# Kernel optimization log

Hardware: AMD Instinct MI355X
Metric: run time of the kernel (lower is better)

Reference implementation:

```python
import jax, jax.numpy as jnp
import numpy as np

# DPLayer config (init kwargs)
MAX_OP = False            # False -> min-plus (shortest path) semiring; null = +inf
MAKE_POS = True           # GraphLayer make_pos: force positive edge weights
NULL = -1e30 if MAX_OP else 1e30   # finite stand-in for +/-inf (grad-safe)
B, H, W = 512, 256, 256


def setup_inputs() -> dict:
    key = jax.random.key(0)
    images = jax.random.normal(key, (B, 1, H, W), dtype=jnp.float32)
    return {"images": images}


def _edge_weights(images):
    # GraphLayer: edge_f('euclidean') on pixel values, made positive via softplus.
    x = images[:, 0, :, :]                       # [B, H, W] node/edge costs theta
    if MAKE_POS:
        x = jax.nn.softplus(x)
    return x


def _dp(theta):
    # V[i,j] = theta[i,j] + comb(V[i-1,j], V[i-1,j-1], V[i,j-1]); comb = min (max_op=False)
    # Row recurrence is solved in parallel via prefix-sum + associative running-min:
    #   A[j] = comb(V[i-1,j], V[i-1,j-1])
    #   V[i,j] = S[j] + runmin_{k<=j}(A[k] - S[k-1]),  S = cumsum(theta row)
    comb = jnp.maximum if MAX_OP else jnp.minimum
    null = jnp.asarray(NULL, theta.dtype)
    b = theta.shape[0]

    v0 = jnp.cumsum(theta[:, 0, :], axis=-1)     # first row: only right moves

    def row_step(vprev, th_row):                 # vprev: [B,W], th_row: [B,W]
        shifted = jnp.concatenate([jnp.full((b, 1), null, theta.dtype), vprev[:, :-1]], axis=1)
        A = comb(vprev, shifted)                 # best of up / up-left
        S = jnp.cumsum(th_row, axis=-1)
        Sprev = jnp.concatenate([jnp.zeros((b, 1), theta.dtype), S[:, :-1]], axis=1)
        V = S + jax.lax.associative_scan(comb, A - Sprev, axis=-1)
        return V, None

    vlast, _ = jax.lax.scan(row_step, v0, jnp.moveaxis(theta[:, 1:, :], 1, 0))
    return vlast[:, -1]                          # path length to (H-1, W-1), [B]


def reference(images):
    theta = _edge_weights(images)
    fake_lengths = _dp(theta)
    return fake_lengths
```

## Files before the change

kernel.cpp:

```cpp
#include <hip/hip_runtime.h>


#define HH 256
#define WW 256
#define CH 16
#define NCH 16
#define NULLV 1e30f

template<int CTRL, int ROWM>
__device__ __forceinline__ float dpp_mov(float x, float oldv) {
    return __builtin_bit_cast(float, __builtin_amdgcn_update_dpp(
        __builtin_bit_cast(int, oldv), __builtin_bit_cast(int, x),
        CTRL, ROWM, 0xF, false));
}

__device__ __forceinline__ float wave_iscan_min(float x) {
    asm volatile(
        "s_nop 1\n\t"
        "v_min_f32_dpp %0, %0, %0 row_shr:1  row_mask:0xf bank_mask:0xf\n\t"
        "s_nop 1\n\t"
        "v_min_f32_dpp %0, %0, %0 row_shr:2  row_mask:0xf bank_mask:0xf\n\t"
        "s_nop 1\n\t"
        "v_min_f32_dpp %0, %0, %0 row_shr:4  row_mask:0xf bank_mask:0xf\n\t"
        "s_nop 1\n\t"
        "v_min_f32_dpp %0, %0, %0 row_shr:8  row_mask:0xf bank_mask:0xf\n\t"
        "s_nop 1\n\t"
        "v_min_f32_dpp %0, %0, %0 row_bcast:15 row_mask:0xa bank_mask:0xf\n\t"
        "s_nop 1\n\t"
        "v_min_f32_dpp %0, %0, %0 row_bcast:31 row_mask:0xc bank_mask:0xf"
        : "+v"(x));
    return x;
}

__device__ __forceinline__ float wave_iscan_add(float x) {
    asm volatile(
        "s_nop 1\n\t"
        "v_add_f32_dpp %0, %0, %0 row_shr:1  row_mask:0xf bank_mask:0xf bound_ctrl:0\n\t"
        "s_nop 1\n\t"
        "v_add_f32_dpp %0, %0, %0 row_shr:2  row_mask:0xf bank_mask:0xf bound_ctrl:0\n\t"
        "s_nop 1\n\t"
        "v_add_f32_dpp %0, %0, %0 row_shr:4  row_mask:0xf bank_mask:0xf bound_ctrl:0\n\t"
        "s_nop 1\n\t"
        "v_add_f32_dpp %0, %0, %0 row_shr:8  row_mask:0xf bank_mask:0xf bound_ctrl:0\n\t"
        "s_nop 1\n\t"
        "v_add_f32_dpp %0, %0, %0 row_bcast:15 row_mask:0xa bank_mask:0xf bound_ctrl:0\n\t"
        "s_nop 1\n\t"
        "v_add_f32_dpp %0, %0, %0 row_bcast:31 row_mask:0xc bank_mask:0xf bound_ctrl:0"
        : "+v"(x));
    return x;
}

__device__ __forceinline__ float softplus_f(float x) {
    float ax = fabsf(x);
    float t  = __expf(-ax);
    return fmaxf(x, 0.0f) + __logf(1.0f + t);
}

__device__ __forceinline__ float4 prep_row(float4 c) {
    float t0 = softplus_f(c.x);
    float t1 = t0 + softplus_f(c.y);
    float t2 = t1 + softplus_f(c.z);
    float t3 = t2 + softplus_f(c.w);
    float s    = wave_iscan_add(t3);
    float soff = dpp_mov<0x138, 0xF>(s, 0.0f);
    return make_float4(soff + t0, soff + t1, soff + t2, soff + t3);
}

template<int NR>
__device__ __forceinline__ void load_rows(const float4* gp, int r0, float4* L) {
#pragma unroll
    for (int i = 0; i < NR; ++i) L[i] = gp[(size_t)(r0 + i) * 64];
}

template<int NR>
__device__ __forceinline__ void prep_store(const float4* L, float* dst, int lane) {
#pragma unroll
    for (int i = 0; i < NR; ++i)
        *reinterpret_cast<float4*>(&dst[i * WW + lane * 4]) = prep_row(L[i]);
}

template<int NR>
__device__ __forceinline__ void prep_run(const float4* gp, int row0,
                                         float* base0, float* base1, int lane) {
    float4 L[NR];
    load_rows<NR>(gp, CH + row0, L);
    __syncthreads();
    for (int k = 1; k < NCH; ++k) {
        float4 N[NR];
        if (k + 1 < NCH) load_rows<NR>(gp, (k + 1) * CH + row0, N);
        prep_store<NR>(L, (k & 1) ? base1 : base0, lane);
        __syncthreads();
        if (k + 1 < NCH) {
#pragma unroll
            for (int i = 0; i < NR; ++i) L[i] = N[i];
        }
    }
}

__global__ __launch_bounds__(512, 1) void dp_kernel(const float* __restrict__ img,
                                                    float* __restrict__ out) {
    const int tid = threadIdx.x;
    const int wid = tid >> 6;
    const int lane = tid & 63;

    __shared__ __align__(16) float sbuf[2][2][CH][WW];

    const int imgi = (wid < 2) ? wid : ((wid - 2) & 1);
    const float* gbase = img + (size_t)(2 * blockIdx.x + imgi) * HH * WW;
    const float4* gp = reinterpret_cast<const float4*>(gbase) + lane;

    if (wid < 2) {
        {
            float4 C[4];
            load_rows<4>(gp, 0, C);
            prep_store<4>(C, &sbuf[imgi][0][0][0], lane);
        }
        __syncthreads();
        __builtin_amdgcn_s_setprio(1);

        float v0, v1, v2, v3;
        auto row_step = [&](const float4& S) {
            float soff = dpp_mov<0x138, 0xF>(S.w, 0.0f);
            float vm1  = dpp_mov<0x138, 0xF>(v3, NULLV);
            float B0 = fminf(v0, vm1) - soff;
            float B1 = fminf(v1, v0) - S.x;
            float B2 = fminf(v2, v1) - S.y;
            float B3 = fminf(v3, v2) - S.z;
            float m1 = fminf(B0, B1);
            float p  = fminf(B2, B3);
            float m2 = fminf(m1, B2);
            float m3 = fminf(m1, p);
            float mm   = wave_iscan_min(m3);
            float moff = dpp_mov<0x138, 0xF>(mm, NULLV);
            v0 = S.x + fminf(moff, B0);
            v1 = S.y + fminf(moff, m1);
            v2 = S.z + fminf(moff, m2);
            v3 = S.w + fminf(moff, m3);
        };

#define RD8(P, buf, r0)                                                  \
    P##0 = *reinterpret_cast<const float4*>(&(buf)[(r0) + 0][lane * 4]); \
    P##1 = *reinterpret_cast<const float4*>(&(buf)[(r0) + 1][lane * 4]); \
    P##2 = *reinterpret_cast<const float4*>(&(buf)[(r0) + 2][lane * 4]); \
    P##3 = *reinterpret_cast<const float4*>(&(buf)[(r0) + 3][lane * 4]); \
    P##4 = *reinterpret_cast<const float4*>(&(buf)[(r0) + 4][lane * 4]); \
    P##5 = *reinterpret_cast<const float4*>(&(buf)[(r0) + 5][lane * 4]); \
    P##6 = *reinterpret_cast<const float4*>(&(buf)[(r0) + 6][lane * 4]); \
    P##7 = *reinterpret_cast<const float4*>(&(buf)[(r0) + 7][lane * 4]);
#define ST8(P)                                                           \
    row_step(P##0); row_step(P##1); row_step(P##2); row_step(P##3);      \
    row_step(P##4); row_step(P##5); row_step(P##6); row_step(P##7);

        float4 A0, A1, A2, A3, A4, A5, A6, A7;
        float4 B0, B1, B2, B3, B4, B5, B6, B7;

        {
            const float(*buf)[WW] = sbuf[imgi][0];
            RD8(A, buf, 0); RD8(B, buf, 8);
            v0 = A0.x; v1 = A0.y; v2 = A0.z; v3 = A0.w;
            row_step(A1); row_step(A2); row_step(A3);
            row_step(A4); row_step(A5); row_step(A6); row_step(A7);
            ST8(B);
        }
        for (int k = 1; k < NCH; ++k) {
            __syncthreads();
            const float(*buf)[WW] = sbuf[imgi][k & 1];
            RD8(A, buf, 0); RD8(B, buf, 8);
            ST8(A);
            ST8(B);
        }
#undef RD8
#undef ST8
        if (lane == 63) out[2 * blockIdx.x + imgi] = v3;
    } else {
        const int pw = (wid - 2) >> 1;
        {
            float4 C[4];
            load_rows<4>(gp, 4 + 4 * pw, C);
            prep_store<4>(C, &sbuf[imgi][0][4 + 4 * pw][0], lane);
        }
        const int row0 = (pw == 0) ? 0 : (pw == 1) ? 6 : 11;
        float* b0 = &sbuf[imgi][0][row0][0];
        float* b1 = &sbuf[imgi][1][row0][0];
        if (pw == 0) prep_run<6>(gp, row0, b0, b1, lane);
        else         prep_run<5>(gp, row0, b0, b1, lane);
    }
}

extern "C" void kernel_launch(void* const* d_in, const int* in_sizes, int n_in,
                              void* d_out, int out_size, void* d_ws, size_t ws_size,
                              hipStream_t stream) {
    const float* img = (const float*)d_in[0];
    float* out = (float*)d_out;
    dp_kernel<<<out_size / 2, 512, 0, stream>>>(img, out);
}
```

Measured before the change: 39.94 us.

## Process one image per block with six producer waves and two blocks per CU

Restructures the kernel so each block handles a single image with one DP wave (wave 3) and six softplus/prefix-sum producer waves, instead of two images with two DP waves and six producers. Shared memory is halved and launch bounds change to 448 threads with 2 blocks per CU, doubling the grid. The intent is finer-grained scheduling and more producer throughput per DP wave so the serial row recurrence is less starved. The cost is more blocks, more barriers per image, and possible register pressure under the tighter occupancy bound.

Result: faster. 38.43 us (median of 2 runs) (-3.8%).

```diff
diff --git a/kernel.cpp b/kernel.cpp
--- a/kernel.cpp
+++ b/kernel.cpp
@@ -97,23 +97,22 @@
     }
 }
 
-__global__ __launch_bounds__(512, 1) void dp_kernel(const float* __restrict__ img,
+__global__ __launch_bounds__(448, 2) void dp_kernel(const float* __restrict__ img,
                                                     float* __restrict__ out) {
     const int tid = threadIdx.x;
     const int wid = tid >> 6;
     const int lane = tid & 63;
 
-    __shared__ __align__(16) float sbuf[2][2][CH][WW];
+    __shared__ __align__(16) float sbuf[2][CH][WW];
 
-    const int imgi = (wid < 2) ? wid : ((wid - 2) & 1);
-    const float* gbase = img + (size_t)(2 * blockIdx.x + imgi) * HH * WW;
+    const float* gbase = img + (size_t)blockIdx.x * HH * WW;
     const float4* gp = reinterpret_cast<const float4*>(gbase) + lane;
 
-    if (wid < 2) {
+    if (wid == 3) {
         {
-            float4 C[4];
-            load_rows<4>(gp, 0, C);
-            prep_store<4>(C, &sbuf[imgi][0][0][0], lane);
+            float4 C[2];
+            load_rows<2>(gp, 0, C);
+            prep_store<2>(C, &sbuf[0][0][0], lane);
         }
         __syncthreads();
         __builtin_amdgcn_s_setprio(1);
@@ -155,7 +154,7 @@
         float4 B0, B1, B2, B3, B4, B5, B6, B7;
 
         {
-            const float(*buf)[WW] = sbuf[imgi][0];
+            const float(*buf)[WW] = sbuf[0];
             RD8(A, buf, 0); RD8(B, buf, 8);
             v0 = A0.x; v1 = A0.y; v2 = A0.z; v3 = A0.w;
             row_step(A1); row_step(A2); row_step(A3);
@@ -164,26 +163,28 @@
         }
         for (int k = 1; k < NCH; ++k) {
             __syncthreads();
-            const float(*buf)[WW] = sbuf[imgi][k & 1];
+            const float(*buf)[WW] = sbuf[k & 1];
             RD8(A, buf, 0); RD8(B, buf, 8);
             ST8(A);
             ST8(B);
         }
 #undef RD8
 #undef ST8
-        if (lane == 63) out[2 * blockIdx.x + imgi] = v3;
+        if (lane == 63) out[blockIdx.x] = v3;
     } else {
-        const int pw = (wid - 2) >> 1;
-        {
-            float4 C[4];
-            load_rows<4>(gp, 4 + 4 * pw, C);
-            prep_store<4>(C, &sbuf[imgi][0][4 + 4 * pw][0], lane);
-        }
-        const int row0 = (pw == 0) ? 0 : (pw == 1) ? 6 : 11;
-        float* b0 = &sbuf[imgi][0][row0][0];
-        float* b1 = &sbuf[imgi][1][row0][0];
-        if (pw == 0) prep_run<6>(gp, row0, b0, b1, lane);
-        else         prep_run<5>(gp, row0, b0, b1, lane);
+        if (wid == 0) { float4 C[3]; load_rows<3>(gp,  2, C); prep_store<3>(C, &sbuf[0][ 2][0], lane); }
+        else if (wid == 1) { float4 C[3]; load_rows<3>(gp,  5, C); prep_store<3>(C, &sbuf[0][ 5][0], lane); }
+        else if (wid == 2) { float4 C[3]; load_rows<3>(gp,  8, C); prep_store<3>(C, &sbuf[0][ 8][0], lane); }
+        else if (wid == 4) { float4 C[2]; load_rows<2>(gp, 11, C); prep_store<2>(C, &sbuf[0][11][0], lane); }
+        else if (wid == 5) { float4 C[2]; load_rows<2>(gp, 13, C); prep_store<2>(C, &sbuf[0][13][0], lane); }
+        else               { float4 C[1]; load_rows<1>(gp, 15, C); prep_store<1>(C, &sbuf[0][15][0], lane); }
+
+        if (wid == 0)      prep_run<3>(gp,  0, &sbuf[0][ 0][0], &sbuf[1][ 0][0], lane);
+        else if (wid == 1) prep_run<3>(gp,  3, &sbuf[0][ 3][0], &sbuf[1][ 3][0], lane);
+        else if (wid == 2) prep_run<3>(gp,  6, &sbuf[0][ 6][0], &sbuf[1][ 6][0], lane);
+        else if (wid == 4) prep_run<3>(gp,  9, &sbuf[0][ 9][0], &sbuf[1][ 9][0], lane);
+        else if (wid == 5) prep_run<2>(gp, 12, &sbuf[0][12][0], &sbuf[1][12][0], lane);
+        else               prep_run<2>(gp, 14, &sbuf[0][14][0], &sbuf[1][14][0], lane);
     }
 }
 
@@ -192,5 +193,5 @@
                               hipStream_t stream) {
     const float* img = (const float*)d_in[0];
     float* out = (float*)d_out;
-    dp_kernel<<<out_size / 2, 512, 0, stream>>>(img, out);
+    dp_kernel<<<out_size, 448, 0, stream>>>(img, out);
 }
```

## Pack three images per block with one chain wave per image

Applied to the files above, without the earlier changes.

Each workgroup now processes three images instead of two, using 768 threads. Waves whose index has low two bits equal to 3 run the serial DP chains, and the other nine waves do softplus/prefix-sum preprocessing into a three-slot shared buffer. The grid shrinks to ceil(B/3) blocks, and an image-index clamp handles the tail, where one image is computed twice. This trades CU-level parallelism for more per-block packing. The chain waves may also share one SIMD under a wave-index-mod-4 placement, which would make them compete for issue slots.

Result: slower. 51.50 us (+28.9%).

```diff
diff --git a/kernel.cpp b/kernel.cpp
--- a/kernel.cpp
+++ b/kernel.cpp
@@ -97,23 +97,28 @@
     }
 }
 
-__global__ __launch_bounds__(512, 1) void dp_kernel(const float* __restrict__ img,
-                                                    float* __restrict__ out) {
+__global__ __launch_bounds__(768, 1) void dp_kernel(const float* __restrict__ img,
+                                                    float* __restrict__ out,
+                                                    int nimg) {
     const int tid = threadIdx.x;
     const int wid = tid >> 6;
     const int lane = tid & 63;
 
-    __shared__ __align__(16) float sbuf[2][2][CH][WW];
-
-    const int imgi = (wid < 2) ? wid : ((wid - 2) & 1);
-    const float* gbase = img + (size_t)(2 * blockIdx.x + imgi) * HH * WW;
+    __shared__ __align__(16) float sbuf[3][2][CH][WW];
+
+    const bool is_chain = ((wid & 3) == 3);
+    const int slot = is_chain ? (wid >> 2) : (wid & 3);
+    const int pw   = is_chain ? -1 : (wid >> 2);
+    int imgi = 3 * blockIdx.x + slot;
+    if (imgi >= nimg) imgi = nimg - 1;
+    const float* gbase = img + (size_t)imgi * HH * WW;
     const float4* gp = reinterpret_cast<const float4*>(gbase) + lane;
 
-    if (wid < 2) {
+    if (is_chain) {
         {
             float4 C[4];
             load_rows<4>(gp, 0, C);
-            prep_store<4>(C, &sbuf[imgi][0][0][0], lane);
+            prep_store<4>(C, &sbuf[slot][0][0][0], lane);
         }
         __syncthreads();
         __builtin_amdgcn_s_setprio(1);
@@ -155,7 +160,7 @@
         float4 B0, B1, B2, B3, B4, B5, B6, B7;
 
         {
-            const float(*buf)[WW] = sbuf[imgi][0];
+            const float(*buf)[WW] = sbuf[slot][0];
             RD8(A, buf, 0); RD8(B, buf, 8);
             v0 = A0.x; v1 = A0.y; v2 = A0.z; v3 = A0.w;
             row_step(A1); row_step(A2); row_step(A3);
@@ -164,24 +169,23 @@
         }
         for (int k = 1; k < NCH; ++k) {
             __syncthreads();
-            const float(*buf)[WW] = sbuf[imgi][k & 1];
+            const float(*buf)[WW] = sbuf[slot][k & 1];
             RD8(A, buf, 0); RD8(B, buf, 8);
             ST8(A);
             ST8(B);
         }
 #undef RD8
 #undef ST8
-        if (lane == 63) out[2 * blockIdx.x + imgi] = v3;
+        if (lane == 63) out[imgi] = v3;
     } else {
-        const int pw = (wid - 2) >> 1;
         {
             float4 C[4];
             load_rows<4>(gp, 4 + 4 * pw, C);
-            prep_store<4>(C, &sbuf[imgi][0][4 + 4 * pw][0], lane);
+            prep_store<4>(C, &sbuf[slot][0][4 + 4 * pw][0], lane);
         }
         const int row0 = (pw == 0) ? 0 : (pw == 1) ? 6 : 11;
-        float* b0 = &sbuf[imgi][0][row0][0];
-        float* b1 = &sbuf[imgi][1][row0][0];
+        float* b0 = &sbuf[slot][0][row0][0];
+        float* b1 = &sbuf[slot][1][row0][0];
         if (pw == 0) prep_run<6>(gp, row0, b0, b1, lane);
         else         prep_run<5>(gp, row0, b0, b1, lane);
     }
@@ -192,5 +196,6 @@
                               hipStream_t stream) {
     const float* img = (const float*)d_in[0];
     float* out = (float*)d_out;
-    dp_kernel<<<out_size / 2, 512, 0, stream>>>(img, out);
-}
+    int nblocks = (out_size + 2) / 3;
+    dp_kernel<<<nblocks, 768, 0, stream>>>(img, out, out_size);
+}
```
